# Optimization experiments

Measured on AMD Instinct MI355X. Metric: run time of the kernel, lower is better.

## Reference

```python
import jax, jax.numpy as jnp
import numpy as np

U, NB, I, D = 20000, 10000, 40000, 64
L = 2          # num_layers
H = 64         # fusion hidden
M = 40         # max bundle size
BATCH, K = 8192, 2
DEG_UI, DEG_UB = 30, 20


def _sym_block(r, c, nA, nB):
    """Build symmetric bipartite block [[0, A],[A^T, 0]] with laplace normalization."""
    rows = np.concatenate([r, c + nA])
    cols = np.concatenate([c + nA, r])
    n = nA + nB
    deg = np.bincount(rows, minlength=n).astype(np.float64)
    inv = 1.0 / (np.sqrt(deg) + 1e-8)
    vals = (inv[rows] * inv[cols]).astype(np.float32)
    return rows.astype(np.int32), cols.astype(np.int32), vals


def setup_inputs() -> dict:
    rng = np.random.default_rng(0)
    ui_r = np.repeat(np.arange(U), DEG_UI)
    ui_c = rng.integers(0, I, U * DEG_UI)
    il_rows, il_cols, il_vals = _sym_block(ui_r, ui_c, U, I)
    ub_r = np.repeat(np.arange(U), DEG_UB)
    ub_c = rng.integers(0, NB, U * DEG_UB)
    bl_rows, bl_cols, bl_vals = _sym_block(ub_r, ub_c, U, NB)
    lengths = rng.integers(10, M + 1, NB)
    bundle_item_ids = rng.integers(0, I, (NB, M)).astype(np.int32)
    bundle_item_mask = (np.arange(M)[None, :] < lengths[:, None])

    key = jax.random.key(0)
    ks = jax.random.split(key, 8)

    def xavier(k, shape):
        std = np.sqrt(2.0 / (shape[0] + shape[1])).astype(np.float32)
        return jax.random.normal(k, shape, dtype=jnp.float32) * std

    return {
        'users_feature': xavier(ks[0], (U, D)),
        'items_feature': xavier(ks[1], (I, D)),
        'bundles_feature': xavier(ks[2], (NB, D)),
        'fw1': xavier(ks[3], (2 * D, H)),
        'fb1': jnp.zeros((H,), jnp.float32),
        'fw2': xavier(ks[4], (H, 1)),
        'fb2': jnp.zeros((1,), jnp.float32),
        'il_rows': jnp.asarray(il_rows), 'il_cols': jnp.asarray(il_cols), 'il_vals': jnp.asarray(il_vals),
        'bl_rows': jnp.asarray(bl_rows), 'bl_cols': jnp.asarray(bl_cols), 'bl_vals': jnp.asarray(bl_vals),
        'bundle_item_ids': jnp.asarray(bundle_item_ids),
        'bundle_item_mask': jnp.asarray(bundle_item_mask),
        'users': jax.random.randint(ks[5], (BATCH,), 0, U, dtype=jnp.int32),
        'bundles': jax.random.randint(ks[6], (BATCH, K), 0, NB, dtype=jnp.int32),
    }


def _spmm(rows, cols, vals, x, n):
    return jax.ops.segment_sum(vals[:, None] * x[cols], rows, num_segments=n)


def _propagate(rows, cols, vals, feat_a, feat_b):
    # one_propagate: L rounds of spmm, /(layer+2), L2-normalize, then sum over layers
    na = feat_a.shape[0]
    n = na + feat_b.shape[0]
    f = jnp.concatenate([feat_a, feat_b], axis=0)
    acc = f
    for layer in range(L):
        f = _spmm(rows, cols, vals, f, n) / (layer + 2)
        norm = jnp.maximum(jnp.linalg.norm(f, axis=1, keepdims=True), 1e-12)
        acc = acc + f / norm
    return acc[:na], acc[na:]


def reference(users_feature, items_feature, bundles_feature, fw1, fb1, fw2, fb2,
              il_rows, il_cols, il_vals, bl_rows, bl_cols, bl_vals,
              bundle_item_ids, bundle_item_mask, users, bundles):
    IL_u, IL_i = _propagate(il_rows, il_cols, il_vals, users_feature, items_feature)
    BL_u, BL_b = _propagate(bl_rows, bl_cols, bl_vals, users_feature, bundles_feature)

    q = IL_u[users]                          # [B, D] item-level user rep
    ids = bundle_item_ids[bundles]           # [B, K, M]
    msk = bundle_item_mask[bundles]          # [B, K, M]
    it = IL_i[ids]                           # [B, K, M, D]

    # user-conditioned dot attention over bundle items, masked softmax
    logits = jnp.einsum('bd,bkmd->bkm', q, it)
    logits = jnp.where(msk, logits, jnp.float32(-1e9))
    w = jax.nn.softmax(logits, axis=-1)
    il_bundle = jnp.einsum('bkm,bkmd->bkd', w, it)   # attended item-level bundle rep

    il_score = jnp.einsum('bd,bkd->bk', q, il_bundle)
    bl_u = BL_u[users]
    bl_score = jnp.einsum('bd,bkd->bk', bl_u, BL_b[bundles])

    # user-specific view fusion gate
    gate_in = jnp.concatenate([q, bl_u], axis=-1)        # [B, 2D]
    g = jax.nn.sigmoid(jax.nn.relu(gate_in @ fw1 + fb1) @ fw2 + fb2)  # [B, 1]
    pred = g * il_score + (1.0 - g) * bl_score           # [B, K]
    return pred
```

## Files before the change

### kernel.cpp

```cpp
#include <hip/hip_runtime.h>
#include <hip/hip_bf16.h>
#include <math.h>


typedef unsigned short ushortT;
#define CHUNK 8192

__device__ __forceinline__ float wSum(float v) {
#pragma unroll
    for (int o = 32; o >= 1; o >>= 1) v += __shfl_xor(v, o, 64);
    return v;
}
__device__ __forceinline__ float wMax(float v) {
#pragma unroll
    for (int o = 32; o >= 1; o >>= 1) v = fmaxf(v, __shfl_xor(v, o, 64));
    return v;
}
__device__ __forceinline__ float bf2f(ushortT u) {
    return __uint_as_float(((unsigned int)u) << 16);
}
__device__ __forceinline__ ushortT f2bf(float f) {
    unsigned int x = __float_as_uint(f);
    return (ushortT)((x + 0x7fffu + ((x >> 16) & 1u)) >> 16);
}
__device__ __forceinline__ void up2(unsigned int u, float& lo, float& hi) {
    lo = __uint_as_float(u << 16);
    hi = __uint_as_float(u & 0xffff0000u);
}
__device__ __forceinline__ unsigned int pk2(float lo, float hi) {
    return ((unsigned int)f2bf(hi) << 16) | f2bf(lo);
}

__global__ void zero_ints(int* __restrict__ p, int n) {
    int i = blockIdx.x * blockDim.x + threadIdx.x;
    if (i < n) p[i] = 0;
}

__global__ void deg_store2(const int* __restrict__ colsA, const float* __restrict__ valsA,
                           int nAA, int halfA, float suA, int* __restrict__ cntA,
                           const int* __restrict__ colsB, const float* __restrict__ valsB,
                           int nAB, int halfB, float suB, int* __restrict__ cntB) {
    int i = blockIdx.x * blockDim.x + threadIdx.x;
    if (i < halfA) {
        float invc = valsA[i] * suA;
        float x = 1.f / invc - 1e-8f;
        cntA[colsA[i] - nAA] = (int)(x * x + 0.5f);
    } else if (i < halfA + halfB) {
        int j = i - halfA;
        float invc = valsB[j] * suB;
        float x = 1.f / invc - 1e-8f;
        cntB[colsB[j] - nAB] = (int)(x * x + 0.5f);
    }
}

__global__ void scan1_2(const int* __restrict__ cntA, int nA_, int nbA, int* __restrict__ partA,
                        const int* __restrict__ cntB, int nB_, int* __restrict__ partB) {
    int blk = blockIdx.x;
    const int* cnt; int n; int* part; int cb;
    if (blk < nbA) { cnt = cntA; n = nA_; part = partA; cb = blk; }
    else           { cnt = cntB; n = nB_; part = partB; cb = blk - nbA; }
    int t = threadIdx.x;
    int i = cb * 256 + t;
    int v = (i < n) ? cnt[i] : 0;
#pragma unroll
    for (int o = 32; o >= 1; o >>= 1) v += __shfl_xor(v, o, 64);
    __shared__ int sm[4];
    if ((t & 63) == 0) sm[t >> 6] = v;
    __syncthreads();
    if (t == 0) part[cb] = sm[0] + sm[1] + sm[2] + sm[3];
}

__global__ void scan2_2(int* __restrict__ partA, int nbA, int* __restrict__ partB, int nbB) {
    int* part = (blockIdx.x == 0) ? partA : partB;
    int nb = (blockIdx.x == 0) ? nbA : nbB;
    __shared__ int sm[256];
    int t = threadIdx.x;
    int v = (t < nb) ? part[t] : 0;
    sm[t] = v;
    __syncthreads();
    for (int off = 1; off < 256; off <<= 1) {
        int x = (t >= off) ? sm[t - off] : 0;
        __syncthreads();
        sm[t] += x;
        __syncthreads();
    }
    if (t < nb) part[t] = sm[t] - v;
}

__global__ void scan3_2(const int* __restrict__ cntA, const int* __restrict__ partA,
                        int* __restrict__ ofsA, int* __restrict__ curA, int nA_, int nbA,
                        const int* __restrict__ cntB, const int* __restrict__ partB,
                        int* __restrict__ ofsB, int* __restrict__ curB, int nB_) {
    int blk = blockIdx.x;
    const int *cnt, *part; int *ofs, *cur; int n, cb;
    if (blk < nbA) { cnt = cntA; part = partA; ofs = ofsA; cur = curA; n = nA_; cb = blk; }
    else           { cnt = cntB; part = partB; ofs = ofsB; cur = curB; n = nB_; cb = blk - nbA; }
    __shared__ int sm[256];
    int t = threadIdx.x;
    int i = cb * 256 + t;
    int v = (i < n) ? cnt[i] : 0;
    sm[t] = v;
    __syncthreads();
    for (int off = 1; off < 256; off <<= 1) {
        int x = (t >= off) ? sm[t - off] : 0;
        __syncthreads();
        sm[t] += x;
        __syncthreads();
    }
    int excl = sm[t] - v + part[cb];
    if (i < n) {
        ofs[i] = excl;
        cur[i] = excl;
        if (i == n - 1) ofs[n] = excl + v;
    }
}

__global__ void p1hist(const int* __restrict__ colsA, int halfA, int nblkA, int cpbA, int nAA,
                       int* __restrict__ histTA,
                       const int* __restrict__ colsB, int halfB, int nblkB, int cpbB, int nAB,
                       int* __restrict__ histTB) {
    __shared__ int h[256];
    int blk = blockIdx.x, t = threadIdx.x;
    const int* cols; int half, nblk, cpb, nA0, k; int* histT;
    if (blk < nblkA) { cols = colsA; half = halfA; nblk = nblkA; cpb = cpbA; nA0 = nAA; histT = histTA; k = blk; }
    else             { cols = colsB; half = halfB; nblk = nblkB; cpb = cpbB; nA0 = nAB; histT = histTB; k = blk - nblkA; }
    h[t] = 0;
    __syncthreads();
    int s = k * CHUNK, e = min(s + CHUNK, half);
    for (int i = s + t; i < e; i += 256) atomicAdd(&h[(cols[i] - nA0) / cpb], 1);
    __syncthreads();
    histT[t * nblk + k] = h[t];
}

__global__ void p1scat(const int* __restrict__ rowsA, const int* __restrict__ colsA,
                       int halfA, int nblkA, int cpbA, int nAA,
                       const int* __restrict__ hsA, unsigned int* __restrict__ pairA,
                       const int* __restrict__ rowsB, const int* __restrict__ colsB,
                       int halfB, int nblkB, int cpbB, int nAB,
                       const int* __restrict__ hsB, unsigned int* __restrict__ pairB) {
    __shared__ int cur[256];
    int blk = blockIdx.x, t = threadIdx.x;
    const int *rows, *cols, *hs; int half, nblk, cpb, nA0, k; unsigned int* pair;
    if (blk < nblkA) { rows = rowsA; cols = colsA; hs = hsA; pair = pairA;
                       half = halfA; nblk = nblkA; cpb = cpbA; nA0 = nAA; k = blk; }
    else             { rows = rowsB; cols = colsB; hs = hsB; pair = pairB;
                       half = halfB; nblk = nblkB; cpb = cpbB; nA0 = nAB; k = blk - nblkA; }
    cur[t] = hs[t * nblk + k];
    __syncthreads();
    int s = k * CHUNK, e = min(s + CHUNK, half);
    for (int i = s + t; i < e; i += 256) {
        int c = cols[i] - nA0;
        int pos = atomicAdd(&cur[c / cpb], 1);
        pair[pos] = ((unsigned int)c << 16) | (unsigned int)rows[i];
    }
}

__global__ void p2scat(const unsigned int* __restrict__ pairA, const int* __restrict__ ofsA,
                       int cpbA, int nColsA, int* __restrict__ tuA,
                       const unsigned int* __restrict__ pairB, const int* __restrict__ ofsB,
                       int cpbB, int nColsB, int* __restrict__ tuB) {
    __shared__ int cur[512];
    int blk = blockIdx.x, t = threadIdx.x;
    const unsigned int* pair; const int* ofs; int cpb, nCols, b; int* tu;
    if (blk < 256) { pair = pairA; ofs = ofsA; cpb = cpbA; nCols = nColsA; tu = tuA; b = blk; }
    else           { pair = pairB; ofs = ofsB; cpb = cpbB; nCols = nColsB; tu = tuB; b = blk - 256; }
    int c0 = b * cpb;
    if (c0 >= nCols) return;
    int c1 = min(c0 + cpb, nCols);
    for (int j = t; j < c1 - c0; j += 256) cur[j] = ofs[c0 + j];
    __syncthreads();
    int s = ofs[c0], e = ofs[c1];
    for (int i = s + t; i < e; i += 256) {
        unsigned int pr = pair[i];
        int pos = atomicAdd(&cur[(pr >> 16) - c0], 1);
        tu[pos] = (int)(pr & 0xffffu);
    }
}

__global__ void scatter2(const int* __restrict__ rowsA, const int* __restrict__ colsA,
                         int nAA, int halfA, int* __restrict__ curA, int* __restrict__ tuA,
                         const int* __restrict__ rowsB, const int* __restrict__ colsB,
                         int nAB, int halfB, int* __restrict__ curB, int* __restrict__ tuB) {
    int i = blockIdx.x * blockDim.x + threadIdx.x;
    if (i < halfA) {
        int c = colsA[i] - nAA;
        int p = atomicAdd(&curA[c], 1);
        tuA[p] = rowsA[i];
    } else if (i < halfA + halfB) {
        int j = i - halfA;
        int c = colsB[j] - nAB;
        int p = atomicAdd(&curB[c], 1);
        tuB[p] = rowsB[j];
    }
}

__global__ void init2(const float* __restrict__ uf, const float* __restrict__ itf,
                      const float* __restrict__ buf,
                      ushortT* __restrict__ f0A, float* __restrict__ accFA, int nA, int nTotA,
                      ushortT* __restrict__ f0B, float* __restrict__ accFB, int nTotB) {
    int idx = blockIdx.x * blockDim.x + threadIdx.x;
    int totA = nTotA * 64;
    if (idx < totA) {
        int r = idx >> 6;
        float v = (r < nA) ? uf[idx] : itf[idx - nA * 64];
        f0A[idx] = f2bf(v);
        accFA[idx] = v;
    } else if (idx < totA + nTotB * 64) {
        int j = idx - totA;
        int r = j >> 6;
        float v = (r < nA) ? uf[j] : buf[j - nA * 64];
        f0B[j] = f2bf(v);
        accFB[j] = v;
    }
}

template <int DEG>
__device__ __forceinline__ void layer8_body(
    const int* __restrict__ cols, const float* __restrict__ vals,
    const int* __restrict__ ofs, const int* __restrict__ tuser,
    const ushortT* __restrict__ f, ushortT* __restrict__ fnext,
    float* __restrict__ accF, ushortT* __restrict__ accOut,
    int row, int p, int nA, int nTot, int deg, float invu, float inv_s, int last) {
    if (row >= nTot) return;
    float a[8] = {0.f, 0.f, 0.f, 0.f, 0.f, 0.f, 0.f, 0.f};
    if (row < nA) {
        const int* cp = cols + (long)row * deg;
        const float* vp = vals + (long)row * deg;
        if constexpr (DEG > 0) {
#pragma unroll 10
            for (int e = 0; e < DEG; ++e) {
                int c = cp[e];
                float vv = vp[e];
                uint4 rv = *(const uint4*)(f + ((long)c << 6) + (p << 3));
                float x0, x1;
                up2(rv.x, x0, x1); a[0] = fmaf(vv, x0, a[0]); a[1] = fmaf(vv, x1, a[1]);
                up2(rv.y, x0, x1); a[2] = fmaf(vv, x0, a[2]); a[3] = fmaf(vv, x1, a[3]);
                up2(rv.z, x0, x1); a[4] = fmaf(vv, x0, a[4]); a[5] = fmaf(vv, x1, a[5]);
                up2(rv.w, x0, x1); a[6] = fmaf(vv, x0, a[6]); a[7] = fmaf(vv, x1, a[7]);
            }
        } else {
#pragma unroll 4
            for (int e = 0; e < deg; ++e) {
                int c = cp[e];
                float vv = vp[e];
                uint4 rv = *(const uint4*)(f + ((long)c << 6) + (p << 3));
                float x0, x1;
                up2(rv.x, x0, x1); a[0] = fmaf(vv, x0, a[0]); a[1] = fmaf(vv, x1, a[1]);
                up2(rv.y, x0, x1); a[2] = fmaf(vv, x0, a[2]); a[3] = fmaf(vv, x1, a[3]);
                up2(rv.z, x0, x1); a[4] = fmaf(vv, x0, a[4]); a[5] = fmaf(vv, x1, a[5]);
                up2(rv.w, x0, x1); a[6] = fmaf(vv, x0, a[6]); a[7] = fmaf(vv, x1, a[7]);
            }
        }
    } else {
        int r2 = row - nA;
        int s = ofs[r2], e2 = ofs[r2 + 1];
#pragma unroll 4
        for (int j = s; j < e2; ++j) {
            int uu = tuser[j];
            uint4 rv = *(const uint4*)(f + ((long)uu << 6) + (p << 3));
            float x0, x1;
            up2(rv.x, x0, x1); a[0] += x0; a[1] += x1;
            up2(rv.y, x0, x1); a[2] += x0; a[3] += x1;
            up2(rv.z, x0, x1); a[4] += x0; a[5] += x1;
            up2(rv.w, x0, x1); a[6] += x0; a[7] += x1;
        }
        float invi = 1.f / (sqrtf((float)(e2 - s)) + 1e-8f);
        float sc = invi * invu;
#pragma unroll
        for (int d = 0; d < 8; ++d) a[d] *= sc;
    }
    float ss = 0.f;
#pragma unroll
    for (int d = 0; d < 8; ++d) {
        a[d] *= inv_s;
        ss = fmaf(a[d], a[d], ss);
    }
    ss += __shfl_xor(ss, 1, 64);
    ss += __shfl_xor(ss, 2, 64);
    ss += __shfl_xor(ss, 4, 64);
    float inv_nrm = 1.f / fmaxf(sqrtf(ss), 1e-12f);
    long base = ((long)row << 6) + (p << 3);
    if (last) {
        float4 c0 = *(const float4*)(accF + base);
        float4 c1 = *(const float4*)(accF + base + 4);
        uint4 ob;
        ob.x = pk2(c0.x + a[0] * inv_nrm, c0.y + a[1] * inv_nrm);
        ob.y = pk2(c0.z + a[2] * inv_nrm, c0.w + a[3] * inv_nrm);
        ob.z = pk2(c1.x + a[4] * inv_nrm, c1.y + a[5] * inv_nrm);
        ob.w = pk2(c1.z + a[6] * inv_nrm, c1.w + a[7] * inv_nrm);
        *(uint4*)(accOut + base) = ob;
    } else {
        float4 c0 = *(const float4*)(accF + base);
        float4 c1 = *(const float4*)(accF + base + 4);
        c0.x += a[0] * inv_nrm; c0.y += a[1] * inv_nrm;
        c0.z += a[2] * inv_nrm; c0.w += a[3] * inv_nrm;
        c1.x += a[4] * inv_nrm; c1.y += a[5] * inv_nrm;
        c1.z += a[6] * inv_nrm; c1.w += a[7] * inv_nrm;
        *(float4*)(accF + base) = c0;
        *(float4*)(accF + base + 4) = c1;
        uint4 fb;
        fb.x = pk2(a[0], a[1]);
        fb.y = pk2(a[2], a[3]);
        fb.z = pk2(a[4], a[5]);
        fb.w = pk2(a[6], a[7]);
        *(uint4*)(fnext + base) = fb;
    }
}

template <int DA, int DB>
__global__ void __launch_bounds__(256) layer8_fused(
    const int* colsA, const float* valsA, const int* ofsA, const int* tuA,
    const ushortT* fA, ushortT* fnA, float* accFA, ushortT* accOutA,
    int nAA, int nTotA, int degA, float invuA,
    const int* colsB, const float* valsB, const int* ofsB, const int* tuB,
    const ushortT* fB, ushortT* fnB, float* accFB, ushortT* accOutB,
    int nAB, int nTotB, int degB, float invuB,
    float inv_s, int last) {
    int gw = (blockIdx.x * blockDim.x + threadIdx.x) >> 6;
    int lane = threadIdx.x & 63;
    int oct = lane >> 3, p = lane & 7;
    int wA = (nTotA + 7) >> 3;
    int wB = (nTotB + 7) >> 3;
    if (gw < wA) {
        layer8_body<DA>(colsA, valsA, ofsA, tuA, fA, fnA, accFA, accOutA,
                        gw * 8 + oct, p, nAA, nTotA, degA, invuA, inv_s, last);
    } else if (gw < wA + wB) {
        layer8_body<DB>(colsB, valsB, ofsB, tuB, fB, fnB, accFB, accOutB,
                        (gw - wA) * 8 + oct, p, nAB, nTotB, degB, invuB, inv_s, last);
    }
}

template <int MM>
__global__ void __launch_bounds__(256) score_kernel_t(
    const ushortT* __restrict__ accIL, const ushortT* __restrict__ accBL,
    const int* __restrict__ bitem, const unsigned char* __restrict__ mask8,
    const int* __restrict__ users, const int* __restrict__ bundles,
    const float* __restrict__ fw1, const float* __restrict__ fb1,
    const float* __restrict__ fw2, const float* __restrict__ fb2,
    float* __restrict__ out, int U, int K, int B) {
    int b = (blockIdx.x * blockDim.x + threadIdx.x) >> 6;
    int lane = threadIdx.x & 63;
    if (b >= B) return;
    bool mu8 = (mask8[1] != 0);
    const int* m32 = (const int*)mask8;

    int u = users[b];
    const ushortT* qrow = accIL + ((long)u << 6);
    float q = bf2f(qrow[lane]);
    float blu = bf2f(accBL[((long)u << 6) + lane]);

    int pos = lane & 7;
    uint4 qv = *(const uint4*)(qrow + (pos << 3));
    float q8[8];
    up2(qv.x, q8[0], q8[1]);
    up2(qv.y, q8[2], q8[3]);
    up2(qv.z, q8[4], q8[5]);
    up2(qv.w, q8[6], q8[7]);

    float h0 = fb1[lane], h1 = 0.f, h2 = 0.f, h3 = 0.f;
#pragma unroll
    for (int i = 0; i < 64; i += 4) {
        h0 = fmaf(__shfl(q, i, 64),     fw1[i * 64 + lane],       h0);
        h1 = fmaf(__shfl(q, i + 1, 64), fw1[(i + 1) * 64 + lane], h1);
        h2 = fmaf(__shfl(q, i + 2, 64), fw1[(i + 2) * 64 + lane], h2);
        h3 = fmaf(__shfl(q, i + 3, 64), fw1[(i + 3) * 64 + lane], h3);
    }
#pragma unroll
    for (int i = 0; i < 64; i += 4) {
        h0 = fmaf(__shfl(blu, i, 64),     fw1[(64 + i) * 64 + lane],     h0);
        h1 = fmaf(__shfl(blu, i + 1, 64), fw1[(64 + i + 1) * 64 + lane], h1);
        h2 = fmaf(__shfl(blu, i + 2, 64), fw1[(64 + i + 2) * 64 + lane], h2);
        h3 = fmaf(__shfl(blu, i + 3, 64), fw1[(64 + i + 3) * 64 + lane], h3);
    }
    float h = fmaxf((h0 + h1) + (h2 + h3), 0.f);
    float gd = wSum(h * fw2[lane]) + fb2[0];
    float g = 1.f / (1.f + __expf(-gd));

    for (int k = 0; k < K; ++k) {
        int bd = bundles[b * K + k];
        float blb = bf2f(accBL[((long)(U + bd)) * 64 + lane]);
        long ib = (long)bd * MM;
        int idl = (lane < MM) ? bitem[ib + lane] : 0;
        bool mv = (lane < MM) ? (mu8 ? (mask8[ib + lane] != 0) : (m32[ib + lane] != 0))
                              : false;
        unsigned long long vmask = __ballot(mv);

        float el = -1e30f, lr = 0.f;
#pragma unroll
        for (int i = 0; i < MM / 8; ++i) {
            int id = __shfl(idl, 8 * i + (lane >> 3), 64);
            uint4 rv = *(const uint4*)(accIL + (((long)(U + id)) << 6) + (pos << 3));
            float a0, a1, s;
            up2(rv.x, a0, a1);
            s = fmaf(q8[0], a0, q8[1] * a1);
            up2(rv.y, a0, a1);
            s = fmaf(q8[2], a0, fmaf(q8[3], a1, s));
            up2(rv.z, a0, a1);
            s = fmaf(q8[4], a0, fmaf(q8[5], a1, s));
            up2(rv.w, a0, a1);
            s = fmaf(q8[6], a0, fmaf(q8[7], a1, s));
            s += __shfl_xor(s, 1, 64);
            s += __shfl_xor(s, 2, 64);
            s += __shfl_xor(s, 4, 64);
            float v = __shfl(s, (lane & 7) << 3, 64);
            if ((lane >> 3) == i) {
                lr = v;
                el = ((vmask >> lane) & 1ull) ? v : -1e9f;
            }
        }
        float bl = wSum(blu * blb);
        float maxl = wMax(el);
        float pe = __expf(el - maxl);
        float sum = wSum(pe);
        float il = wSum(pe * lr) / sum;
        if (lane == 0) out[b * K + k] = g * il + (1.f - g) * bl;
    }
}

__global__ void __launch_bounds__(256) score_kernel_gen(
    const ushortT* __restrict__ accIL, const ushortT* __restrict__ accBL,
    const int* __restrict__ bitem, const unsigned char* __restrict__ mask8,
    const int* __restrict__ users, const int* __restrict__ bundles,
    const float* __restrict__ fw1, const float* __restrict__ fb1,
    const float* __restrict__ fw2, const float* __restrict__ fb2,
    float* __restrict__ out, int U, int M, int K, int B) {
    int b = (blockIdx.x * blockDim.x + threadIdx.x) >> 6;
    int lane = threadIdx.x & 63;
    if (b >= B) return;
    bool mu8 = (mask8[1] != 0);
    const int* m32 = (const int*)mask8;
    int u = users[b];
    float q = bf2f(accIL[((long)u << 6) + lane]);
    float blu = bf2f(accBL[((long)u << 6) + lane]);
    float h = fb1[lane];
#pragma unroll 8
    for (int i = 0; i < 64; ++i) h = fmaf(__shfl(q, i, 64), fw1[i * 64 + lane], h);
#pragma unroll 8
    for (int i = 0; i < 64; ++i) h = fmaf(__shfl(blu, i, 64), fw1[(64 + i) * 64 + lane], h);
    h = fmaxf(h, 0.f);
    float gd = wSum(h * fw2[lane]) + fb2[0];
    float g = 1.f / (1.f + __expf(-gd));
    for (int k = 0; k < K; ++k) {
        int bd = bundles[b * K + k];
        float blb = bf2f(accBL[((long)(U + bd)) * 64 + lane]);
        float bl = wSum(blu * blb);
        long ib = (long)bd * M;
        int idl = (lane < M) ? bitem[ib + lane] : 0;
        bool mv = (lane < M) ? (mu8 ? (mask8[ib + lane] != 0) : (m32[ib + lane] != 0))
                             : false;
        unsigned long long vmask = __ballot(mv);
        float el = -1e30f, lr = 0.f;
#pragma unroll 8
        for (int m = 0; m < M; ++m) {
            int id = __shfl(idl, m, 64);
            float it = bf2f(accIL[((long)(U + id)) * 64 + lane]);
            float l = wSum(q * it);
            float lm = ((vmask >> m) & 1ull) ? l : -1e9f;
            if (lane == m) { el = lm; lr = l; }
        }
        float maxl = wMax(el);
        float pe = __expf(el - maxl);
        float sum = wSum(pe);
        float il = wSum(pe * lr) / sum;
        if (lane == 0) out[b * K + k] = g * il + (1.f - g) * bl;
    }
}

extern "C" void kernel_launch(void* const* d_in, const int* in_sizes, int n_in,
                              void* d_out, int out_size, void* d_ws, size_t ws_size,
                              hipStream_t stream) {
    const float* users_feature   = (const float*)d_in[0];
    const float* items_feature   = (const float*)d_in[1];
    const float* bundles_feature = (const float*)d_in[2];
    const float* fw1 = (const float*)d_in[3];
    const float* fb1 = (const float*)d_in[4];
    const float* fw2 = (const float*)d_in[5];
    const float* fb2 = (const float*)d_in[6];
    const int*   il_rows = (const int*)d_in[7];
    const int*   il_cols = (const int*)d_in[8];
    const float* il_vals = (const float*)d_in[9];
    const int*   bl_rows = (const int*)d_in[10];
    const int*   bl_cols = (const int*)d_in[11];
    const float* bl_vals = (const float*)d_in[12];
    const int*   bitem   = (const int*)d_in[13];
    const unsigned char* bmask = (const unsigned char*)d_in[14];
    const int*   users   = (const int*)d_in[15];
    const int*   bundles = (const int*)d_in[16];

    const int D = 64;
    int U  = in_sizes[0] / D;
    int I  = in_sizes[1] / D;
    int NB = in_sizes[2] / D;
    int nnzIL = in_sizes[7];
    int nnzBL = in_sizes[10];
    int degUI = (nnzIL / 2) / U;
    int degUB = (nnzBL / 2) / U;
    int M = in_sizes[13] / NB;
    int BATCH = in_sizes[15];
    int K = in_sizes[16] / BATCH;
    int nIL = U + I;
    int nBL = U + NB;
    int halfIL = U * degUI;
    int halfBL = U * degUB;

    char* wsB = (char*)d_ws;
    size_t off = 0;
    auto alc = [&](size_t bytes) -> void* {
        void* p = wsB + off;
        off = (off + bytes + 255) & ~(size_t)255;
        return p;
    };
    float*   accF_IL = (float*)alc((size_t)nIL * 64 * 4);
    float*   accF_BL = (float*)alc((size_t)nBL * 64 * 4);
    ushortT* accILbf = (ushortT*)alc((size_t)nIL * 64 * 2);
    ushortT* accBLbf = (ushortT*)alc((size_t)nBL * 64 * 2);
    ushortT* f0A = (ushortT*)alc((size_t)nIL * 64 * 2);
    ushortT* f1A = (ushortT*)alc((size_t)nIL * 64 * 2);
    ushortT* f0B = (ushortT*)alc((size_t)nBL * 64 * 2);
    ushortT* f1B = (ushortT*)alc((size_t)nBL * 64 * 2);
    int* ofsIL = (int*)alc((size_t)(I + 1) * 4);
    int* tuIL  = (int*)alc((size_t)halfIL * 4);
    int* ofsBL = (int*)alc((size_t)(NB + 1) * 4);
    int* tuBL  = (int*)alc((size_t)halfBL * 4);
    int* cnt   = (int*)alc((size_t)(I + NB) * 4);
    int* cur   = (int*)alc((size_t)(I + NB) * 4);
    int* partA = (int*)alc(256 * 4);
    int* partB = (int*)alc(256 * 4);
    int* cntIL = cnt,  *cntBL = cnt + I;
    int* curIL = cur,  *curBL = cur + I;

    int nblkA = (halfIL + CHUNK - 1) / CHUNK;
    int nblkB = (halfBL + CHUNK - 1) / CHUNK;
    int cpbA = (I + 255) / 256;
    int cpbB = (NB + 255) / 256;
    int LA = 256 * nblkA, LB = 256 * nblkB;
    unsigned int* pairIL = (unsigned int*)alc((size_t)halfIL * 4);
    unsigned int* pairBL = (unsigned int*)alc((size_t)halfBL * 4);
    int* histTA  = (int*)alc((size_t)LA * 4);
    int* histSA  = (int*)alc((size_t)(LA + 1) * 4);
    int* curSA   = (int*)alc((size_t)LA * 4);
    int* histTB  = (int*)alc((size_t)LB * 4);
    int* histSB  = (int*)alc((size_t)(LB + 1) * 4);
    int* curSB   = (int*)alc((size_t)LB * 4);
    int* partA2  = (int*)alc(256 * 4);
    int* partB2  = (int*)alc(256 * 4);

    zero_ints<<<(I + NB + 255) / 256, 256, 0, stream>>>(cnt, I + NB);
    float suA = sqrtf((float)degUI) + 1e-8f;
    float suB = sqrtf((float)degUB) + 1e-8f;
    deg_store2<<<(halfIL + halfBL + 255) / 256, 256, 0, stream>>>(
        il_cols, il_vals, U, halfIL, suA, cntIL,
        bl_cols, bl_vals, U, halfBL, suB, cntBL);
    int nbA = (I + 255) / 256, nbB = (NB + 255) / 256;
    scan1_2<<<nbA + nbB, 256, 0, stream>>>(cntIL, I, nbA, partA, cntBL, NB, partB);
    scan2_2<<<2, 256, 0, stream>>>(partA, nbA, partB, nbB);
    scan3_2<<<nbA + nbB, 256, 0, stream>>>(cntIL, partA, ofsIL, curIL, I, nbA,
                                           cntBL, partB, ofsBL, curBL, NB);

    bool fast = (I < 65536) && (NB < 65536) && (U < 65536) &&
                (cpbA <= 512) && (cpbB <= 512) &&
                (nblkA >= 1) && (nblkB >= 1) && (nblkA <= 256) && (nblkB <= 256);
    if (fast) {
        p1hist<<<nblkA + nblkB, 256, 0, stream>>>(
            il_cols, halfIL, nblkA, cpbA, U, histTA,
            bl_cols, halfBL, nblkB, cpbB, U, histTB);
        scan1_2<<<nblkA + nblkB, 256, 0, stream>>>(histTA, LA, nblkA, partA2, histTB, LB, partB2);
        scan2_2<<<2, 256, 0, stream>>>(partA2, nblkA, partB2, nblkB);
        scan3_2<<<nblkA + nblkB, 256, 0, stream>>>(histTA, partA2, histSA, curSA, LA, nblkA,
                                                   histTB, partB2, histSB, curSB, LB);
        p1scat<<<nblkA + nblkB, 256, 0, stream>>>(
            il_rows, il_cols, halfIL, nblkA, cpbA, U, histSA, pairIL,
            bl_rows, bl_cols, halfBL, nblkB, cpbB, U, histSB, pairBL);
        p2scat<<<512, 256, 0, stream>>>(pairIL, ofsIL, cpbA, I, tuIL,
                                        pairBL, ofsBL, cpbB, NB, tuBL);
    } else {
        scatter2<<<(halfIL + halfBL + 255) / 256, 256, 0, stream>>>(
            il_rows, il_cols, U, halfIL, curIL, tuIL,
            bl_rows, bl_cols, U, halfBL, curBL, tuBL);
    }

    int elemsTot = (nIL + nBL) * 64;
    init2<<<(elemsTot + 255) / 256, 256, 0, stream>>>(
        users_feature, items_feature, bundles_feature,
        f0A, accF_IL, U, nIL, f0B, accF_BL, nBL);
    float invuA = 1.f / suA;
    float invuB = 1.f / suB;
    int wavesTot = ((nIL + 7) >> 3) + ((nBL + 7) >> 3);
    int lgrid = (wavesTot * 64 + 255) / 256;
    if (degUI == 30 && degUB == 20) {
        layer8_fused<30, 20><<<lgrid, 256, 0, stream>>>(
            il_cols, il_vals, ofsIL, tuIL, f0A, f1A, accF_IL, accILbf, U, nIL, degUI, invuA,
            bl_cols, bl_vals, ofsBL, tuBL, f0B, f1B, accF_BL, accBLbf, U, nBL, degUB, invuB,
            0.5f, 0);
        layer8_fused<30, 20><<<lgrid, 256, 0, stream>>>(
            il_cols, il_vals, ofsIL, tuIL, f1A, f0A, accF_IL, accILbf, U, nIL, degUI, invuA,
            bl_cols, bl_vals, ofsBL, tuBL, f1B, f0B, accF_BL, accBLbf, U, nBL, degUB, invuB,
            1.f / 3.f, 1);
    } else {
        layer8_fused<0, 0><<<lgrid, 256, 0, stream>>>(
            il_cols, il_vals, ofsIL, tuIL, f0A, f1A, accF_IL, accILbf, U, nIL, degUI, invuA,
            bl_cols, bl_vals, ofsBL, tuBL, f0B, f1B, accF_BL, accBLbf, U, nBL, degUB, invuB,
            0.5f, 0);
        layer8_fused<0, 0><<<lgrid, 256, 0, stream>>>(
            il_cols, il_vals, ofsIL, tuIL, f1A, f0A, accF_IL, accILbf, U, nIL, degUI, invuA,
            bl_cols, bl_vals, ofsBL, tuBL, f1B, f0B, accF_BL, accBLbf, U, nBL, degUB, invuB,
            1.f / 3.f, 1);
    }

    if (M == 40) {
        score_kernel_t<40><<<(BATCH * 64 + 255) / 256, 256, 0, stream>>>(
            accILbf, accBLbf, bitem, bmask, users, bundles, fw1, fb1, fw2, fb2,
            (float*)d_out, U, K, BATCH);
    } else {
        score_kernel_gen<<<(BATCH * 64 + 255) / 256, 256, 0, stream>>>(
            accILbf, accBLbf, bitem, bmask, users, bundles, fw1, fb1, fw2, fb2,
            (float*)d_out, U, M, K, BATCH);
    }
}
```

Baseline: 175.3 us.

## Fuse CSR-build prep kernels and drop fp32 accumulator buffer in propagation

Merges zeroing with the bf16 feature init, merges degree recovery with the per-chunk column histogram, and collapses the two three-pass scans into two four-way kernels where each block sums its prefix partials directly. The fp32 running accumulator is removed. Layer 1 now stores only the bf16 features and a per-row norm, and layer 2 rebuilds the sum from the original fp32 inputs, the stored layer-1 features times their norm, and its own result. This cuts kernel launches and the full fp32 read/write traffic. The cost is an extra bf16 feature read in the last layer, a redundant partial-prefix sum in every scan block, and layer-1 contributions rounded through bf16.

```diff
diff --git a/kernel.cpp b/kernel.cpp
--- a/kernel.cpp
+++ b/kernel.cpp
@@ -31,35 +31,62 @@
     return ((unsigned int)f2bf(hi) << 16) | f2bf(lo);
 }
 
-__global__ void zero_ints(int* __restrict__ p, int n) {
-    int i = blockIdx.x * blockDim.x + threadIdx.x;
-    if (i < n) p[i] = 0;
-}
-
-__global__ void deg_store2(const int* __restrict__ colsA, const float* __restrict__ valsA,
-                           int nAA, int halfA, float suA, int* __restrict__ cntA,
-                           const int* __restrict__ colsB, const float* __restrict__ valsB,
-                           int nAB, int halfB, float suB, int* __restrict__ cntB) {
-    int i = blockIdx.x * blockDim.x + threadIdx.x;
-    if (i < halfA) {
-        float invc = valsA[i] * suA;
-        float x = 1.f / invc - 1e-8f;
-        cntA[colsA[i] - nAA] = (int)(x * x + 0.5f);
-    } else if (i < halfA + halfB) {
-        int j = i - halfA;
-        float invc = valsB[j] * suB;
-        float x = 1.f / invc - 1e-8f;
-        cntB[colsB[j] - nAB] = (int)(x * x + 0.5f);
-    }
-}
-
-__global__ void scan1_2(const int* __restrict__ cntA, int nA_, int nbA, int* __restrict__ partA,
-                        const int* __restrict__ cntB, int nB_, int* __restrict__ partB) {
-    int blk = blockIdx.x;
+__global__ void init_zero(const float* __restrict__ uf, const float* __restrict__ itf,
+                          const float* __restrict__ buf,
+                          ushortT* __restrict__ f0A, int nA, int nTotA,
+                          ushortT* __restrict__ f0B, int nTotB,
+                          int* __restrict__ cnt, int cntN) {
+    int idx = blockIdx.x * blockDim.x + threadIdx.x;
+    if (idx < cntN) cnt[idx] = 0;
+    int totA = nTotA * 64;
+    if (idx < totA) {
+        int r = idx >> 6;
+        f0A[idx] = f2bf((r < nA) ? uf[idx] : itf[idx - nA * 64]);
+    } else if (idx < totA + nTotB * 64) {
+        int j = idx - totA;
+        int r = j >> 6;
+        f0B[j] = f2bf((r < nA) ? uf[j] : buf[j - nA * 64]);
+    }
+}
+
+__global__ void prep_edges(
+    const int* __restrict__ colsA, const float* __restrict__ valsA,
+    int halfA, int nblkA, int cpbA, int nA0A, float suA,
+    int* __restrict__ cntA, int* __restrict__ histTA,
+    const int* __restrict__ colsB, const float* __restrict__ valsB,
+    int halfB, int nblkB, int cpbB, int nA0B, float suB,
+    int* __restrict__ cntB, int* __restrict__ histTB) {
+    __shared__ int h[256];
+    int blk = blockIdx.x, t = threadIdx.x;
+    const int* cols; const float* vals; int half, nblk, cpb, nA0, k;
+    float su; int *cnt, *histT;
+    if (blk < nblkA) { cols = colsA; vals = valsA; half = halfA; nblk = nblkA; cpb = cpbA;
+                       nA0 = nA0A; su = suA; cnt = cntA; histT = histTA; k = blk; }
+    else             { cols = colsB; vals = valsB; half = halfB; nblk = nblkB; cpb = cpbB;
+                       nA0 = nA0B; su = suB; cnt = cntB; histT = histTB; k = blk - nblkA; }
+    h[t] = 0;
+    __syncthreads();
+    int s = k * CHUNK, e = min(s + CHUNK, half);
+    for (int i = s + t; i < e; i += 256) {
+        int c = cols[i] - nA0;
+        float x = 1.f / (vals[i] * su) - 1e-8f;
+        cnt[c] = (int)(x * x + 0.5f);
+        atomicAdd(&h[c / cpb], 1);
+    }
+    __syncthreads();
+    histT[t * nblk + k] = h[t];
+}
+
+__global__ void scan1_4(const int* c0, int n0, int nb0, int* p0,
+                        const int* c1, int n1, int nb1, int* p1,
+                        const int* c2, int n2, int nb2, int* p2,
+                        const int* c3, int n3, int nb3, int* p3) {
+    int blk = blockIdx.x, t = threadIdx.x;
     const int* cnt; int n; int* part; int cb;
-    if (blk < nbA) { cnt = cntA; n = nA_; part = partA; cb = blk; }
-    else           { cnt = cntB; n = nB_; part = partB; cb = blk - nbA; }
-    int t = threadIdx.x;
+    if (blk < nb0)                 { cnt = c0; n = n0; part = p0; cb = blk; }
+    else if (blk < nb0 + nb1)      { cnt = c1; n = n1; part = p1; cb = blk - nb0; }
+    else if (blk < nb0 + nb1 + nb2){ cnt = c2; n = n2; part = p2; cb = blk - nb0 - nb1; }
+    else                           { cnt = c3; n = n3; part = p3; cb = blk - nb0 - nb1 - nb2; }
     int i = cb * 256 + t;
     int v = (i < n) ? cnt[i] : 0;
 #pragma unroll
@@ -70,66 +97,41 @@
     if (t == 0) part[cb] = sm[0] + sm[1] + sm[2] + sm[3];
 }
 
-__global__ void scan2_2(int* __restrict__ partA, int nbA, int* __restrict__ partB, int nbB) {
-    int* part = (blockIdx.x == 0) ? partA : partB;
-    int nb = (blockIdx.x == 0) ? nbA : nbB;
+__global__ void scan3_4(const int* c0, int n0, int nb0, const int* p0, int* o0, int* u0,
+                        const int* c1, int n1, int nb1, const int* p1, int* o1, int* u1,
+                        const int* c2, int n2, int nb2, const int* p2, int* o2,
+                        const int* c3, int n3, int nb3, const int* p3, int* o3) {
     __shared__ int sm[256];
-    int t = threadIdx.x;
-    int v = (t < nb) ? part[t] : 0;
+    int blk = blockIdx.x, t = threadIdx.x;
+    const int *cnt, *part; int *ofs, *cur; int n, cb, tail;
+    if (blk < nb0)                 { cnt = c0; n = n0; part = p0; ofs = o0; cur = u0; cb = blk; tail = 1; }
+    else if (blk < nb0 + nb1)      { cnt = c1; n = n1; part = p1; ofs = o1; cur = u1; cb = blk - nb0; tail = 1; }
+    else if (blk < nb0 + nb1 + nb2){ cnt = c2; n = n2; part = p2; ofs = o2; cur = 0; cb = blk - nb0 - nb1; tail = 0; }
+    else                           { cnt = c3; n = n3; part = p3; ofs = o3; cur = 0; cb = blk - nb0 - nb1 - nb2; tail = 0; }
+    sm[t] = (t < cb) ? part[t] : 0;
+    __syncthreads();
+    for (int o = 128; o >= 1; o >>= 1) {
+        if (t < o) sm[t] += sm[t + o];
+        __syncthreads();
+    }
+    int base = sm[0];
+    __syncthreads();
+    int i = cb * 256 + t;
+    int v = (i < n) ? cnt[i] : 0;
     sm[t] = v;
     __syncthreads();
-    for (int off = 1; off < 256; off <<= 1) {
-        int x = (t >= off) ? sm[t - off] : 0;
+    for (int o = 1; o < 256; o <<= 1) {
+        int x = (t >= o) ? sm[t - o] : 0;
         __syncthreads();
         sm[t] += x;
         __syncthreads();
     }
-    if (t < nb) part[t] = sm[t] - v;
-}
-
-__global__ void scan3_2(const int* __restrict__ cntA, const int* __restrict__ partA,
-                        int* __restrict__ ofsA, int* __restrict__ curA, int nA_, int nbA,
-                        const int* __restrict__ cntB, const int* __restrict__ partB,
-                        int* __restrict__ ofsB, int* __restrict__ curB, int nB_) {
-    int blk = blockIdx.x;
-    const int *cnt, *part; int *ofs, *cur; int n, cb;
-    if (blk < nbA) { cnt = cntA; part = partA; ofs = ofsA; cur = curA; n = nA_; cb = blk; }
-    else           { cnt = cntB; part = partB; ofs = ofsB; cur = curB; n = nB_; cb = blk - nbA; }
-    __shared__ int sm[256];
-    int t = threadIdx.x;
-    int i = cb * 256 + t;
-    int v = (i < n) ? cnt[i] : 0;
-    sm[t] = v;
-    __syncthreads();
-    for (int off = 1; off < 256; off <<= 1) {
-        int x = (t >= off) ? sm[t - off] : 0;
-        __syncthreads();
-        sm[t] += x;
-        __syncthreads();
-    }
-    int excl = sm[t] - v + part[cb];
+    int excl = sm[t] - v + base;
     if (i < n) {
         ofs[i] = excl;
-        cur[i] = excl;
-        if (i == n - 1) ofs[n] = excl + v;
-    }
-}
-
-__global__ void p1hist(const int* __restrict__ colsA, int halfA, int nblkA, int cpbA, int nAA,
-                       int* __restrict__ histTA,
-                       const int* __restrict__ colsB, int halfB, int nblkB, int cpbB, int nAB,
-                       int* __restrict__ histTB) {
-    __shared__ int h[256];
-    int blk = blockIdx.x, t = threadIdx.x;
-    const int* cols; int half, nblk, cpb, nA0, k; int* histT;
-    if (blk < nblkA) { cols = colsA; half = halfA; nblk = nblkA; cpb = cpbA; nA0 = nAA; histT = histTA; k = blk; }
-    else             { cols = colsB; half = halfB; nblk = nblkB; cpb = cpbB; nA0 = nAB; histT = histTB; k = blk - nblkA; }
-    h[t] = 0;
-    __syncthreads();
-    int s = k * CHUNK, e = min(s + CHUNK, half);
-    for (int i = s + t; i < e; i += 256) atomicAdd(&h[(cols[i] - nA0) / cpb], 1);
-    __syncthreads();
-    histT[t * nblk + k] = h[t];
+        if (cur) cur[i] = excl;
+        if (tail && i == n - 1) ofs[n] = excl + v;
+    }
 }
 
 __global__ void p1scat(const int* __restrict__ rowsA, const int* __restrict__ colsA,
@@ -194,33 +196,15 @@
     }
 }
 
-__global__ void init2(const float* __restrict__ uf, const float* __restrict__ itf,
-                      const float* __restrict__ buf,
-                      ushortT* __restrict__ f0A, float* __restrict__ accFA, int nA, int nTotA,
-                      ushortT* __restrict__ f0B, float* __restrict__ accFB, int nTotB) {
-    int idx = blockIdx.x * blockDim.x + threadIdx.x;
-    int totA = nTotA * 64;
-    if (idx < totA) {
-        int r = idx >> 6;
-        float v = (r < nA) ? uf[idx] : itf[idx - nA * 64];
-        f0A[idx] = f2bf(v);
-        accFA[idx] = v;
-    } else if (idx < totA + nTotB * 64) {
-        int j = idx - totA;
-        int r = j >> 6;
-        float v = (r < nA) ? uf[j] : buf[j - nA * 64];
-        f0B[j] = f2bf(v);
-        accFB[j] = v;
-    }
-}
-
-template <int DEG>
+template <int DEG, int LAST>
 __device__ __forceinline__ void layer8_body(
     const int* __restrict__ cols, const float* __restrict__ vals,
     const int* __restrict__ ofs, const int* __restrict__ tuser,
     const ushortT* __restrict__ f, ushortT* __restrict__ fnext,
-    float* __restrict__ accF, ushortT* __restrict__ accOut,
-    int row, int p, int nA, int nTot, int deg, float invu, float inv_s, int last) {
+    float* __restrict__ nrm,
+    const float* __restrict__ origU, const float* __restrict__ origO,
+    ushortT* __restrict__ accOut,
+    int row, int p, int nA, int nTot, int deg, float invu, float inv_s) {
     if (row >= nTot) return;
     float a[8] = {0.f, 0.f, 0.f, 0.f, 0.f, 0.f, 0.f, 0.f};
     if (row < nA) {
@@ -280,53 +264,57 @@
     ss += __shfl_xor(ss, 4, 64);
     float inv_nrm = 1.f / fmaxf(sqrtf(ss), 1e-12f);
     long base = ((long)row << 6) + (p << 3);
-    if (last) {
-        float4 c0 = *(const float4*)(accF + base);
-        float4 c1 = *(const float4*)(accF + base + 4);
-        uint4 ob;
-        ob.x = pk2(c0.x + a[0] * inv_nrm, c0.y + a[1] * inv_nrm);
-        ob.y = pk2(c0.z + a[2] * inv_nrm, c0.w + a[3] * inv_nrm);
-        ob.z = pk2(c1.x + a[4] * inv_nrm, c1.y + a[5] * inv_nrm);
-        ob.w = pk2(c1.z + a[6] * inv_nrm, c1.w + a[7] * inv_nrm);
-        *(uint4*)(accOut + base) = ob;
-    } else {
-        float4 c0 = *(const float4*)(accF + base);
-        float4 c1 = *(const float4*)(accF + base + 4);
-        c0.x += a[0] * inv_nrm; c0.y += a[1] * inv_nrm;
-        c0.z += a[2] * inv_nrm; c0.w += a[3] * inv_nrm;
-        c1.x += a[4] * inv_nrm; c1.y += a[5] * inv_nrm;
-        c1.z += a[6] * inv_nrm; c1.w += a[7] * inv_nrm;
-        *(float4*)(accF + base) = c0;
-        *(float4*)(accF + base + 4) = c1;
+    if constexpr (!LAST) {
+        if (p == 0) nrm[row] = inv_nrm;
         uint4 fb;
         fb.x = pk2(a[0], a[1]);
         fb.y = pk2(a[2], a[3]);
         fb.z = pk2(a[4], a[5]);
         fb.w = pk2(a[6], a[7]);
         *(uint4*)(fnext + base) = fb;
-    }
-}
-
-template <int DA, int DB>
+    } else {
+        const float* op = (row < nA) ? (origU + base)
+                                     : (origO + (((long)(row - nA)) << 6) + (p << 3));
+        float4 c0 = *(const float4*)op;
+        float4 c1 = *(const float4*)(op + 4);
+        float n1 = nrm[row];
+        uint4 f1v = *(const uint4*)(f + base);
+        float x0, x1, x2, x3, x4, x5, x6, x7;
+        up2(f1v.x, x0, x1);
+        up2(f1v.y, x2, x3);
+        up2(f1v.z, x4, x5);
+        up2(f1v.w, x6, x7);
+        uint4 ob;
+        ob.x = pk2(c0.x + x0 * n1 + a[0] * inv_nrm, c0.y + x1 * n1 + a[1] * inv_nrm);
+        ob.y = pk2(c0.z + x2 * n1 + a[2] * inv_nrm, c0.w + x3 * n1 + a[3] * inv_nrm);
+        ob.z = pk2(c1.x + x4 * n1 + a[4] * inv_nrm, c1.y + x5 * n1 + a[5] * inv_nrm);
+        ob.w = pk2(c1.z + x6 * n1 + a[6] * inv_nrm, c1.w + x7 * n1 + a[7] * inv_nrm);
+        *(uint4*)(accOut + base) = ob;
+    }
+}
+
+template <int DA, int DB, int LAST>
 __global__ void __launch_bounds__(256) layer8_fused(
     const int* colsA, const float* valsA, const int* ofsA, const int* tuA,
-    const ushortT* fA, ushortT* fnA, float* accFA, ushortT* accOutA,
+    const ushortT* fA, ushortT* fnA, float* nrmA,
+    const float* origUA, const float* origOA, ushortT* accOutA,
     int nAA, int nTotA, int degA, float invuA,
     const int* colsB, const float* valsB, const int* ofsB, const int* tuB,
-    const ushortT* fB, ushortT* fnB, float* accFB, ushortT* accOutB,
+    const ushortT* fB, ushortT* fnB, float* nrmB,
+    const float* origUB, const float* origOB, ushortT* accOutB,
     int nAB, int nTotB, int degB, float invuB,
-    float inv_s, int last) {
+    float inv_s) {
     int gw = (blockIdx.x * blockDim.x + threadIdx.x) >> 6;
     int lane = threadIdx.x & 63;
     int oct = lane >> 3, p = lane & 7;
     int wA = (nTotA + 7) >> 3;
     int wB = (nTotB + 7) >> 3;
     if (gw < wA) {
-        layer8_body<DA>(colsA, valsA, ofsA, tuA, fA, fnA, accFA, accOutA,
-                        gw * 8 + oct, p, nAA, nTotA, degA, invuA, inv_s, last);
+        layer8_body<DA, LAST>(colsA, valsA, ofsA, tuA, fA, fnA, nrmA, origUA, origOA, accOutA,
+                              gw * 8 + oct, p, nAA, nTotA, degA, invuA, inv_s);
     } else if (gw < wA + wB) {
-        layer8_body<DB>(colsB, valsB, ofsB, tuB, fB, fnB, accFB, accOutB,
-                        (gw - wA) * 8 + oct, p, nAB, nTotB, degB, invuB, inv_s, last);
+        layer8_body<DB, LAST>(colsB, valsB, ofsB, tuB, fB, fnB, nrmB, origUB, origOB, accOutB,
+                              (gw - wA) * 8 + oct, p, nAB, nTotB, degB, invuB, inv_s);
     }
 }
 
@@ -510,22 +498,20 @@
         off = (off + bytes + 255) & ~(size_t)255;
         return p;
     };
-    float*   accF_IL = (float*)alc((size_t)nIL * 64 * 4);
-    float*   accF_BL = (float*)alc((size_t)nBL * 64 * 4);
     ushortT* accILbf = (ushortT*)alc((size_t)nIL * 64 * 2);
     ushortT* accBLbf = (ushortT*)alc((size_t)nBL * 64 * 2);
     ushortT* f0A = (ushortT*)alc((size_t)nIL * 64 * 2);
     ushortT* f1A = (ushortT*)alc((size_t)nIL * 64 * 2);
     ushortT* f0B = (ushortT*)alc((size_t)nBL * 64 * 2);
     ushortT* f1B = (ushortT*)alc((size_t)nBL * 64 * 2);
+    float* nrmA = (float*)alc((size_t)nIL * 4);
+    float* nrmB = (float*)alc((size_t)nBL * 4);
     int* ofsIL = (int*)alc((size_t)(I + 1) * 4);
     int* tuIL  = (int*)alc((size_t)halfIL * 4);
     int* ofsBL = (int*)alc((size_t)(NB + 1) * 4);
     int* tuBL  = (int*)alc((size_t)halfBL * 4);
     int* cnt   = (int*)alc((size_t)(I + NB) * 4);
     int* cur   = (int*)alc((size_t)(I + NB) * 4);
-    int* partA = (int*)alc(256 * 4);
-    int* partB = (int*)alc(256 * 4);
     int* cntIL = cnt,  *cntBL = cnt + I;
     int* curIL = cur,  *curBL = cur + I;
 
@@ -536,38 +522,44 @@
     int LA = 256 * nblkA, LB = 256 * nblkB;
     unsigned int* pairIL = (unsigned int*)alc((size_t)halfIL * 4);
     unsigned int* pairBL = (unsigned int*)alc((size_t)halfBL * 4);
-    int* histTA  = (int*)alc((size_t)LA * 4);
-    int* histSA  = (int*)alc((size_t)(LA + 1) * 4);
-    int* curSA   = (int*)alc((size_t)LA * 4);
-    int* histTB  = (int*)alc((size_t)LB * 4);
-    int* histSB  = (int*)alc((size_t)(LB + 1) * 4);
-    int* curSB   = (int*)alc((size_t)LB * 4);
-    int* partA2  = (int*)alc(256 * 4);
-    int* partB2  = (int*)alc(256 * 4);
-
-    zero_ints<<<(I + NB + 255) / 256, 256, 0, stream>>>(cnt, I + NB);
+    int* histTA = (int*)alc((size_t)LA * 4);
+    int* histSA = (int*)alc((size_t)(LA + 1) * 4);
+    int* histTB = (int*)alc((size_t)LB * 4);
+    int* histSB = (int*)alc((size_t)(LB + 1) * 4);
+    int* part0  = (int*)alc(256 * 4);
+    int* part1  = (int*)alc(256 * 4);
+    int* part2  = (int*)alc(256 * 4);
+    int* part3  = (int*)alc(256 * 4);
+
     float suA = sqrtf((float)degUI) + 1e-8f;
     float suB = sqrtf((float)degUB) + 1e-8f;
-    deg_store2<<<(halfIL + halfBL + 255) / 256, 256, 0, stream>>>(
-        il_cols, il_vals, U, halfIL, suA, cntIL,
-        bl_cols, bl_vals, U, halfBL, suB, cntBL);
-    int nbA = (I + 255) / 256, nbB = (NB + 255) / 256;
-    scan1_2<<<nbA + nbB, 256, 0, stream>>>(cntIL, I, nbA, partA, cntBL, NB, partB);
-    scan2_2<<<2, 256, 0, stream>>>(partA, nbA, partB, nbB);
-    scan3_2<<<nbA + nbB, 256, 0, stream>>>(cntIL, partA, ofsIL, curIL, I, nbA,
-                                           cntBL, partB, ofsBL, curBL, NB);
+
+    int elemsTot = (nIL + nBL) * 64;
+    int izN = elemsTot > (I + NB) ? elemsTot : (I + NB);
+    init_zero<<<(izN + 255) / 256, 256, 0, stream>>>(
+        users_feature, items_feature, bundles_feature,
+        f0A, U, nIL, f0B, nBL, cnt, I + NB);
+
+    prep_edges<<<nblkA + nblkB, 256, 0, stream>>>(
+        il_cols, il_vals, halfIL, nblkA, cpbA, U, suA, cntIL, histTA,
+        bl_cols, bl_vals, halfBL, nblkB, cpbB, U, suB, cntBL, histTB);
+
+    int nb0 = (I + 255) / 256, nb1 = (NB + 255) / 256;
+    int nb2 = nblkA, nb3 = nblkB;
+    scan1_4<<<nb0 + nb1 + nb2 + nb3, 256, 0, stream>>>(
+        cntIL, I, nb0, part0, cntBL, NB, nb1, part1,
+        histTA, LA, nb2, part2, histTB, LB, nb3, part3);
+    scan3_4<<<nb0 + nb1 + nb2 + nb3, 256, 0, stream>>>(
+        cntIL, I, nb0, part0, ofsIL, curIL,
+        cntBL, NB, nb1, part1, ofsBL, curBL,
+        histTA, LA, nb2, part2, histSA,
+        histTB, LB, nb3, part3, histSB);
 
     bool fast = (I < 65536) && (NB < 65536) && (U < 65536) &&
                 (cpbA <= 512) && (cpbB <= 512) &&
+                (nb0 <= 256) && (nb1 <= 256) &&
                 (nblkA >= 1) && (nblkB >= 1) && (nblkA <= 256) && (nblkB <= 256);
     if (fast) {
-        p1hist<<<nblkA + nblkB, 256, 0, stream>>>(
-            il_cols, halfIL, nblkA, cpbA, U, histTA,
-            bl_cols, halfBL, nblkB, cpbB, U, histTB);
-        scan1_2<<<nblkA + nblkB, 256, 0, stream>>>(histTA, LA, nblkA, partA2, histTB, LB, partB2);
-        scan2_2<<<2, 256, 0, stream>>>(partA2, nblkA, partB2, nblkB);
-        scan3_2<<<nblkA + nblkB, 256, 0, stream>>>(histTA, partA2, histSA, curSA, LA, nblkA,
-                                                   histTB, partB2, histSB, curSB, LB);
         p1scat<<<nblkA + nblkB, 256, 0, stream>>>(
             il_rows, il_cols, halfIL, nblkA, cpbA, U, histSA, pairIL,
             bl_rows, bl_cols, halfBL, nblkB, cpbB, U, histSB, pairBL);
@@ -579,32 +571,32 @@
             bl_rows, bl_cols, U, halfBL, curBL, tuBL);
     }
 
-    int elemsTot = (nIL + nBL) * 64;
-    init2<<<(elemsTot + 255) / 256, 256, 0, stream>>>(
-        users_feature, items_feature, bundles_feature,
-        f0A, accF_IL, U, nIL, f0B, accF_BL, nBL);
     float invuA = 1.f / suA;
     float invuB = 1.f / suB;
     int wavesTot = ((nIL + 7) >> 3) + ((nBL + 7) >> 3);
     int lgrid = (wavesTot * 64 + 255) / 256;
     if (degUI == 30 && degUB == 20) {
-        layer8_fused<30, 20><<<lgrid, 256, 0, stream>>>(
-            il_cols, il_vals, ofsIL, tuIL, f0A, f1A, accF_IL, accILbf, U, nIL, degUI, invuA,
-            bl_cols, bl_vals, ofsBL, tuBL, f0B, f1B, accF_BL, accBLbf, U, nBL, degUB, invuB,
-            0.5f, 0);
-        layer8_fused<30, 20><<<lgrid, 256, 0, stream>>>(
-            il_cols, il_vals, ofsIL, tuIL, f1A, f0A, accF_IL, accILbf, U, nIL, degUI, invuA,
-            bl_cols, bl_vals, ofsBL, tuBL, f1B, f0B, accF_BL, accBLbf, U, nBL, degUB, invuB,
-            1.f / 3.f, 1);
+        layer8_fused<30, 20, 0><<<lgrid, 256, 0, stream>>>(
+            il_cols, il_vals, ofsIL, tuIL, f0A, f1A, nrmA, users_feature, items_feature, accILbf,
+            U, nIL, degUI, invuA,
+            bl_cols, bl_vals, ofsBL, tuBL, f0B, f1B, nrmB, users_feature, bundles_feature, accBLbf,
+            U, nBL, degUB, invuB, 0.5f);
+        layer8_fused<30, 20, 1><<<lgrid, 256, 0, stream>>>(
+            il_cols, il_vals, ofsIL, tuIL, f1A, f0A, nrmA, users_feature, items_feature, accILbf,
+            U, nIL, degUI, invuA,
+            bl_cols, bl_vals, ofsBL, tuBL, f1B, f0B, nrmB, users_feature, bundles_feature, accBLbf,
+            U, nBL, degUB, invuB, 1.f / 3.f);
     } else {
-        layer8_fused<0, 0><<<lgrid, 256, 0, stream>>>(
-            il_cols, il_vals, ofsIL, tuIL, f0A, f1A, accF_IL, accILbf, U, nIL, degUI, invuA,
-            bl_cols, bl_vals, ofsBL, tuBL, f0B, f1B, accF_BL, accBLbf, U, nBL, degUB, invuB,
-            0.5f, 0);
-        layer8_fused<0, 0><<<lgrid, 256, 0, stream>>>(
-            il_cols, il_vals, ofsIL, tuIL, f1A, f0A, accF_IL, accILbf, U, nIL, degUI, invuA,
-            bl_cols, bl_vals, ofsBL, tuBL, f1B, f0B, accF_BL, accBLbf, U, nBL, degUB, invuB,
-            1.f / 3.f, 1);
+        layer8_fused<0, 0, 0><<<lgrid, 256, 0, stream>>>(
+            il_cols, il_vals, ofsIL, tuIL, f0A, f1A, nrmA, users_feature, items_feature, accILbf,
+            U, nIL, degUI, invuA,
+            bl_cols, bl_vals, ofsBL, tuBL, f0B, f1B, nrmB, users_feature, bundles_feature, accBLbf,
+            U, nBL, degUB, invuB, 0.5f);
+        layer8_fused<0, 0, 1><<<lgrid, 256, 0, stream>>>(
+            il_cols, il_vals, ofsIL, tuIL, f1A, f0A, nrmA, users_feature, items_feature, accILbf,
+            U, nIL, degUI, invuA,
+            bl_cols, bl_vals, ofsBL, tuBL, f1B, f0B, nrmB, users_feature, bundles_feature, accBLbf,
+            U, nBL, degUB, invuB, 1.f / 3.f);
     }
 
     if (M == 40) {
```

After: 158.7 us. 1.1x faster.
